# Kernel tuning notes

Hardware: AMD Instinct MI355X
Metric: run time of the kernel (lower is better)

## Reference

```python
import jax, jax.numpy as jnp
from jax import lax
import numpy as np

DIM, HEADS, R = 256, 8, 2
B, H, W = 4, 64, 64
C = DIM // HEADS
SCALE = C ** -0.5


def setup_inputs() -> dict:
    key = jax.random.key(0)
    ks = jax.random.split(key, 6)
    s = 0.02
    x = jax.random.normal(ks[0], (B, DIM, H, W), dtype=jnp.float32)
    Wq = jax.random.normal(ks[1], (DIM, DIM), dtype=jnp.float32) * s
    Wkv = jax.random.normal(ks[2], (2 * DIM, DIM, R, R), dtype=jnp.float32) * s
    Wqb = jax.random.normal(ks[3], (DIM, DIM), dtype=jnp.float32) * s
    Wkvb = jax.random.normal(ks[4], (2 * DIM, DIM), dtype=jnp.float32) * s
    Wout = jax.random.normal(ks[5], (DIM, DIM), dtype=jnp.float32) * s
    return {"x": x, "Wq": Wq, "Wkv": Wkv, "Wqb": Wqb, "Wkvb": Wkvb, "Wout": Wout}


def _conv1x1(Wm, t):
    # 1x1 conv without bias == channel matmul
    return jnp.einsum('oc,bchw->bohw', Wm, t)


def reference(x, Wq, Wkv, Wqb, Wkvb, Wout):
    b, d, h, w = x.shape
    c = d // HEADS
    # ---- spatial-reduction branch ----
    q = _conv1x1(Wq, x)  # [b, d, h, w]
    kv = lax.conv_general_dilated(x, Wkv, (R, R), 'VALID',
                                  dimension_numbers=('NCHW', 'OIHW', 'NCHW'))
    k, v = jnp.split(kv, 2, axis=1)  # each [b, d, h/R, w/R]

    def to_img(t):
        bb, _, hh, ww = t.shape
        return t.reshape(bb, HEADS, c, hh * ww).transpose(0, 1, 3, 2).reshape(bb * HEADS, hh * ww, c)

    qi, ki, vi = to_img(q), to_img(k), to_img(v)
    attn_img = jax.nn.softmax(jnp.einsum('bid,bjd->bij', qi, ki) * SCALE, axis=-1)
    oi = jnp.einsum('bij,bjd->bid', attn_img, vi)  # [(b h), hw, c]
    out_img = oi.reshape(b, HEADS, h * w, c).transpose(0, 1, 3, 2).reshape(b, d, h, w)

    # ---- batch-wise branch ----
    qb = _conv1x1(Wqb, x)
    kvb = _conv1x1(Wkvb, x)
    kb, vb = jnp.split(kvb, 2, axis=1)

    def to_slice(t):
        # 'b (h c) x y -> (x y h) b c'
        return t.reshape(b, HEADS, c, h * w).transpose(3, 1, 0, 2).reshape(h * w * HEADS, b, c)

    qs, ks_, vs = to_slice(qb), to_slice(kb), to_slice(vb)
    attn_b = jax.nn.softmax(jnp.einsum('ibd,icd->ibc', qs, ks_) * SCALE, axis=-1)
    ob = jnp.einsum('ibc,icd->ibd', attn_b, vs)  # [(hw heads), b, c]
    out_batch = ob.reshape(h * w, HEADS, b, c).transpose(2, 1, 3, 0).reshape(b, d, h, w)

    return _conv1x1(Wout, out_img + out_batch)
```

## Files before the change

### kernel.cpp

```cpp
#include <hip/hip_runtime.h>

#define ATTN_SCALE 0.17677669529663687f

typedef __attribute__((ext_vector_type(8))) short bf16x8;
typedef __attribute__((ext_vector_type(4))) float f32x4;
typedef __attribute__((ext_vector_type(16))) float f32x16;

__device__ inline unsigned short f2bf(float x) {
    unsigned int u = __float_as_uint(x);
    unsigned int r = u + 0x7fffu + ((u >> 16) & 1u);
    return (unsigned short)(r >> 16);
}
__device__ inline unsigned int pk2(float lo, float hi) {
    return (unsigned int)f2bf(lo) | ((unsigned int)f2bf(hi) << 16);
}
__device__ inline float bf2f(unsigned int u) { return __uint_as_float(u << 16); }

#define GLDS16(gp, lp) \
    __builtin_amdgcn_global_load_lds((const __attribute__((address_space(1))) void*)(gp), \
                                     (__attribute__((address_space(3))) void*)(lp), 16, 0, 0)

template<int NIT>
__device__ inline void stage_tile_n(const ushort* __restrict__ g, int rstride, int kofs,
                                    ushort* lbase, int w, int lane) {
    const int r0 = w * (NIT * 8);
    #pragma unroll
    for (int u = 0; u < NIT; ++u) {
        const int row  = r0 + u * 8 + (lane >> 3);
        const int slog = (lane & 7) ^ (row & 7);
        GLDS16(g + (size_t)row * rstride + kofs + slog * 8,
               lbase + (size_t)(r0 + u * 8) * 64);
    }
}
__device__ inline void stage_tile(const ushort* __restrict__ g, int rstride, int kofs,
                                  ushort* lbase, int w, int lane) {
    stage_tile_n<4>(g, rstride, kofs, lbase, w, lane);
}

__device__ inline bf16x8 frag_ld(const ushort* t, int row, int slog) {
    return *(const bf16x8*)(t + row * 64 + ((slog ^ (row & 7)) * 8));
}

#define MFMA_STEP(WS_, XS_, WM_, WP_)                                                       \
    _Pragma("unroll")                                                                       \
    for (int kh = 0; kh < 2; ++kh) {                                                        \
        bf16x8 av[4], bvv[4];                                                               \
        _Pragma("unroll")                                                                   \
        for (int fm = 0; fm < 4; ++fm) av[fm]  = frag_ld(WS_, WM_ + fm * 16 + i16, kh * 4 + g); \
        _Pragma("unroll")                                                                   \
        for (int fp = 0; fp < 4; ++fp) bvv[fp] = frag_ld(XS_, WP_ + fp * 16 + i16, kh * 4 + g); \
        _Pragma("unroll")                                                                   \
        for (int fm = 0; fm < 4; ++fm)                                                      \
            _Pragma("unroll")                                                               \
            for (int fp = 0; fp < 4; ++fp)                                                  \
                acc[fm][fp] = __builtin_amdgcn_mfma_f32_16x16x32_bf16(av[fm], bvv[fp],      \
                                                                      acc[fm][fp], 0, 0, 0); \
    }

__global__ __launch_bounds__(256) void cvt_x_fused(
    const float* __restrict__ x, ushort* __restrict__ xbfT, ushort* __restrict__ xcol)
{
    __shared__ float T[128][65];
    const int t  = threadIdx.x;
    const int i2 = blockIdx.x;
    const int c0 = blockIdx.y * 64, bb = blockIdx.z;
    const int p0 = i2 * 128;
    const float* xb = x + ((size_t)bb * 256 + c0) * 4096 + p0;

    {
        const int cc = t >> 2;
        const int pq = (t & 3) * 32;
        #pragma unroll
        for (int u = 0; u < 8; ++u) {
            const float4 v = *(const float4*)&xb[(size_t)cc * 4096 + pq + u * 4];
            T[pq + u * 4 + 0][cc] = v.x; T[pq + u * 4 + 1][cc] = v.y;
            T[pq + u * 4 + 2][cc] = v.z; T[pq + u * 4 + 3][cc] = v.w;
        }
    }
    __syncthreads();

    {
        const int pp = t >> 1, ch = (t & 1) * 32;
        const float* row = &T[pp][ch];
        unsigned int pkv[16];
        #pragma unroll
        for (int u = 0; u < 16; ++u) pkv[u] = pk2(row[2 * u], row[2 * u + 1]);
        ushort* dst = xbfT + ((size_t)bb * 4096 + p0 + pp) * 256 + c0 + ch;
        *(uint4*)&dst[0]  = *(uint4*)&pkv[0];
        *(uint4*)&dst[8]  = *(uint4*)&pkv[4];
        *(uint4*)&dst[16] = *(uint4*)&pkv[8];
        *(uint4*)&dst[24] = *(uint4*)&pkv[12];
    }
    {
        const int j = t >> 3, c8 = (t & 7) * 8;
        unsigned int pkv[16];
        #pragma unroll
        for (int c = 0; c < 8; ++c) {
            pkv[2 * c]     = pk2(T[2 * j][c8 + c],      T[2 * j + 1][c8 + c]);
            pkv[2 * c + 1] = pk2(T[64 + 2 * j][c8 + c], T[65 + 2 * j][c8 + c]);
        }
        ushort* dst = xcol + ((size_t)bb * 1024 + i2 * 32 + j) * 1024 + (size_t)(c0 + c8) * 4;
        *(uint4*)&dst[0]  = *(uint4*)&pkv[0];
        *(uint4*)&dst[8]  = *(uint4*)&pkv[4];
        *(uint4*)&dst[16] = *(uint4*)&pkv[8];
        *(uint4*)&dst[24] = *(uint4*)&pkv[12];
    }
}

__global__ __launch_bounds__(256) void cvt_w_kernel(
    const float* __restrict__ Wq, const float* __restrict__ Wqb,
    const float* __restrict__ Wkvb, const float* __restrict__ Wkv,
    const float* __restrict__ Wout,
    ushort* __restrict__ Wallb, ushort* __restrict__ Wkvbb, ushort* __restrict__ Woutb)
{
    const int id = blockIdx.x * 256 + threadIdx.x;
    const float* src; ushort* dst;
    if (id < 65536) {
        const int m = id >> 6, c4 = (id & 63) * 4;
        src = (m < 256) ? &Wq[(size_t)m * 256 + c4]
            : (m < 512) ? &Wqb[(size_t)(m - 256) * 256 + c4]
                        : &Wkvb[(size_t)(m - 512) * 256 + c4];
        dst = Wallb + (size_t)id * 4;
    } else if (id < 65536 + 131072) {
        const size_t el = (size_t)(id - 65536) * 4;
        src = &Wkv[el]; dst = Wkvbb + el;
    } else if (id < 65536 + 131072 + 16384) {
        const size_t el = (size_t)(id - 65536 - 131072) * 4;
        src = &Wout[el]; dst = Woutb + el;
    } else return;
    const float4 v = *(const float4*)src;
    ushort4 o; o.x = f2bf(v.x); o.y = f2bf(v.y); o.z = f2bf(v.z); o.w = f2bf(v.w);
    *(ushort4*)dst = o;
}

__global__ __launch_bounds__(256) void proj_mfma(
    const ushort* __restrict__ Wallb, const ushort* __restrict__ xbfT,
    ushort* __restrict__ qTb, ushort* __restrict__ qbT, ushort* __restrict__ kvbT)
{
    __shared__ __align__(16) ushort lds[16384];
    ushort* Ws = lds; ushort* Xs = lds + 8192;
    const int tid = threadIdx.x, lane = tid & 63, w = tid >> 6;
    const int g = lane >> 4, i16 = lane & 15;
    const int p0 = blockIdx.x * 128, m0 = blockIdx.y * 128, bb = blockIdx.z;
    const int wm = (w >> 1) * 64, wp = (w & 1) * 64;
    const ushort* Ag = Wallb + (size_t)m0 * 256;
    const ushort* Bg = xbfT + ((size_t)bb * 4096 + p0) * 256;
    f32x4 acc[4][4] = {};
    for (int ks = 0; ks < 4; ++ks) {
        stage_tile(Ag, 256, ks * 64, Ws, w, lane);
        stage_tile(Bg, 256, ks * 64, Xs, w, lane);
        __syncthreads();
        MFMA_STEP(Ws, Xs, wm, wp);
        __syncthreads();
    }
    #pragma unroll
    for (int fp = 0; fp < 4; ++fp) {
        const int p = p0 + wp + fp * 16 + i16;
        #pragma unroll
        for (int fm = 0; fm < 4; ++fm) {
            const int m = m0 + wm + fm * 16 + 4 * g;
            if (m0 < 256) {
                ushort4 v;
                v.x = f2bf(acc[fm][fp][0] * ATTN_SCALE); v.y = f2bf(acc[fm][fp][1] * ATTN_SCALE);
                v.z = f2bf(acc[fm][fp][2] * ATTN_SCALE); v.w = f2bf(acc[fm][fp][3] * ATTN_SCALE);
                *(ushort4*)&qTb[((size_t)bb * 4096 + p) * 256 + m] = v;
            } else if (m0 < 512) {
                ushort4 v;
                v.x = f2bf(acc[fm][fp][0]); v.y = f2bf(acc[fm][fp][1]);
                v.z = f2bf(acc[fm][fp][2]); v.w = f2bf(acc[fm][fp][3]);
                *(ushort4*)&qbT[((size_t)bb * 4096 + p) * 256 + (m - 256)] = v;
            } else {
                ushort4 v;
                v.x = f2bf(acc[fm][fp][0]); v.y = f2bf(acc[fm][fp][1]);
                v.z = f2bf(acc[fm][fp][2]); v.w = f2bf(acc[fm][fp][3]);
                *(ushort4*)&kvbT[((size_t)bb * 4096 + p) * 512 + (m - 512)] = v;
            }
        }
    }
}

__global__ __launch_bounds__(256) void conv_mfma(
    const ushort* __restrict__ Wkvbb, const ushort* __restrict__ xcol,
    ushort* __restrict__ kTb, ushort* __restrict__ vTtb)
{
    __shared__ __align__(16) ushort lds[12288];
    ushort* Ws = lds;
    ushort* Xs = lds + 4096;
    const int tid = threadIdx.x, lane = tid & 63, w = tid >> 6;
    const int g = lane >> 4, i16 = lane & 15;
    const int pp0 = blockIdx.x * 128, m0 = blockIdx.y * 64, bb = blockIdx.z;
    const int wm = (w >> 1) * 32, wp = (w & 1) * 64;
    const ushort* Ag = Wkvbb + (size_t)m0 * 1024;
    const ushort* Bg = xcol + ((size_t)bb * 1024 + pp0) * 1024;
    f32x4 acc[2][4] = {};
    for (int ks = 0; ks < 16; ++ks) {
        stage_tile_n<2>(Ag, 1024, ks * 64, Ws, w, lane);
        stage_tile_n<4>(Bg, 1024, ks * 64, Xs, w, lane);
        __syncthreads();
        #pragma unroll
        for (int kh = 0; kh < 2; ++kh) {
            bf16x8 av[2], bvv[4];
            #pragma unroll
            for (int fm = 0; fm < 2; ++fm) av[fm]  = frag_ld(Ws, wm + fm * 16 + i16, kh * 4 + g);
            #pragma unroll
            for (int fp = 0; fp < 4; ++fp) bvv[fp] = frag_ld(Xs, wp + fp * 16 + i16, kh * 4 + g);
            #pragma unroll
            for (int fm = 0; fm < 2; ++fm)
                #pragma unroll
                for (int fp = 0; fp < 4; ++fp)
                    acc[fm][fp] = __builtin_amdgcn_mfma_f32_16x16x32_bf16(av[fm], bvv[fp],
                                                                          acc[fm][fp], 0, 0, 0);
        }
        __syncthreads();
    }
    if (m0 < 256) {
        #pragma unroll
        for (int fp = 0; fp < 4; ++fp) {
            const int pp = pp0 + wp + fp * 16 + i16;
            #pragma unroll
            for (int fm = 0; fm < 2; ++fm) {
                const int m = m0 + wm + fm * 16 + 4 * g;
                ushort4 v;
                v.x = f2bf(acc[fm][fp][0]); v.y = f2bf(acc[fm][fp][1]);
                v.z = f2bf(acc[fm][fp][2]); v.w = f2bf(acc[fm][fp][3]);
                *(ushort4*)&kTb[((size_t)bb * 1024 + pp) * 256 + m] = v;
            }
        }
    } else {
        ushort (*T)[128] = (ushort(*)[128])lds;
        #pragma unroll
        for (int fm = 0; fm < 2; ++fm)
            #pragma unroll
            for (int fp = 0; fp < 4; ++fp)
                #pragma unroll
                for (int r = 0; r < 4; ++r)
                    T[wm + fm * 16 + 4 * g + r][wp + fp * 16 + i16] = f2bf(acc[fm][fp][r]);
        __syncthreads();
        #pragma unroll
        for (int u = 0; u < 4; ++u) {
            const int chunk = u * 256 + tid;
            const int row = chunk >> 4, slot = chunk & 15;
            const int mg = m0 - 256 + row;
            const int hh = mg >> 5, cc = mg & 31;
            const uint4 val = *(uint4*)&T[row][slot * 8];
            *(uint4*)&vTtb[((size_t)(bb * 8 + hh) * 32 + cc) * 1024 + pp0 + slot * 8] = val;
        }
    }
}

__global__ __launch_bounds__(256) void out_mfma(
    const float* __restrict__ sumT, const ushort* __restrict__ Woutb,
    float* __restrict__ out)
{
    __shared__ __align__(16) ushort lds[16384];
    ushort* Ss = lds; ushort* Wo = lds + 8192;
    const int tid = threadIdx.x, lane = tid & 63, w = tid >> 6;
    const int g = lane >> 4, i16 = lane & 15;
    const int p0 = blockIdx.x * 128, o0 = blockIdx.y * 128, bb = blockIdx.z;
    const int wpp = (w >> 1) * 64, wo = (w & 1) * 64;
    const float* Sg = sumT + ((size_t)bb * 4096 + p0) * 256;
    const ushort* Bgw = Woutb + (size_t)o0 * 256;
    const int srow = tid >> 1, shalf = tid & 1;
    f32x4 acc[4][4] = {};
    for (int ks = 0; ks < 4; ++ks) {
        {
            const float* src = Sg + (size_t)srow * 256 + ks * 64 + shalf * 32;
            #pragma unroll
            for (int jj = 0; jj < 4; ++jj) {
                const float4 f0 = *(const float4*)&src[jj * 8];
                const float4 f1 = *(const float4*)&src[jj * 8 + 4];
                uint4 pk;
                pk.x = pk2(f0.x, f0.y); pk.y = pk2(f0.z, f0.w);
                pk.z = pk2(f1.x, f1.y); pk.w = pk2(f1.z, f1.w);
                const int slog = shalf * 4 + jj;
                const int sp = slog ^ (srow & 7);
                *(uint4*)&Ss[(size_t)srow * 64 + sp * 8] = pk;
            }
        }
        stage_tile(Bgw, 256, ks * 64, Wo, w, lane);
        __syncthreads();
        MFMA_STEP(Ss, Wo, wpp, wo);
        __syncthreads();
    }
    #pragma unroll
    for (int fo = 0; fo < 4; ++fo) {
        const int o = o0 + wo + fo * 16 + i16;
        #pragma unroll
        for (int fp = 0; fp < 4; ++fp) {
            const int p = p0 + wpp + fp * 16 + 4 * g;
            const float4 v = make_float4(acc[fp][fo][0], acc[fp][fo][1],
                                         acc[fp][fo][2], acc[fp][fo][3]);
            *(float4*)&out[(size_t)bb * 1048576 + (size_t)o * 4096 + p] = v;
        }
    }
}

__global__ __launch_bounds__(256) void attn_img_mfma(
    const ushort* __restrict__ qTb, const ushort* __restrict__ kTb,
    const ushort* __restrict__ vTtb, float* __restrict__ sumT)
{
    __shared__ ushort Ks[128][40];
    __shared__ ushort Vts[32][136];
    const int tid  = threadIdx.x;
    const int lane = tid & 63;
    const int wv   = tid >> 6;
    const int q    = lane & 31;
    const int hi   = lane >> 5;
    const int bh   = blockIdx.x;
    const int b    = bh >> 3, h = bh & 7;
    const int q0   = blockIdx.y * 128 + wv * 32;

    bf16x8 qf[2];
    #pragma unroll
    for (int mm = 0; mm < 2; ++mm)
        qf[mm] = *(const bf16x8*)(qTb + ((size_t)(b * 4096 + q0 + q) * 256 + h * 32 + mm * 16 + hi * 8));

    f32x16 o = {};
    float mrun = -3.0e38f, lrun = 0.f;

    const ushort* kg = kTb + (size_t)b * 1024 * 256 + h * 32;
    const ushort* vg = vTtb + (size_t)bh * 32 * 1024;

    for (int kv0 = 0; kv0 < 1024; kv0 += 128) {
        __syncthreads();
        #pragma unroll
        for (int u = 0; u < 2; ++u) {
            const int chunk = tid + u * 256;
            const int r = chunk >> 2, q4 = chunk & 3;
            *(uint4*)&Ks[r][q4 * 8] = *(const uint4*)(kg + (size_t)(kv0 + r) * 256 + q4 * 8);
            const int c = chunk >> 4, sseg = chunk & 15;
            *(uint4*)&Vts[c][sseg * 8] = *(const uint4*)(vg + (size_t)c * 1024 + kv0 + sseg * 8);
        }
        __syncthreads();

        f32x16 s[4];
        #pragma unroll
        for (int t = 0; t < 4; ++t) {
            const bf16x8 k0 = *(const bf16x8*)&Ks[t * 32 + q][hi * 8];
            const bf16x8 k1 = *(const bf16x8*)&Ks[t * 32 + q][16 + hi * 8];
            f32x16 acc = {};
            acc = __builtin_amdgcn_mfma_f32_32x32x16_bf16(k0, qf[0], acc, 0, 0, 0);
            acc = __builtin_amdgcn_mfma_f32_32x32x16_bf16(k1, qf[1], acc, 0, 0, 0);
            s[t] = acc;
        }
        float pmax = -3.0e38f;
        #pragma unroll
        for (int t = 0; t < 4; ++t)
            #pragma unroll
            for (int r = 0; r < 16; ++r) pmax = fmaxf(pmax, s[t][r]);
        {
            float a_ = pmax, b_ = pmax;
            asm volatile("v_permlane32_swap_b32 %0, %1" : "+v"(a_), "+v"(b_));
            pmax = fmaxf(a_, b_);
        }
        const float mnew  = fmaxf(mrun, pmax);
        const float alpha = __expf(mrun - mnew);
        mrun = mnew;
        float ls = 0.f;
        #pragma unroll
        for (int t = 0; t < 4; ++t)
            #pragma unroll
            for (int r = 0; r < 16; ++r) {
                const float p = __expf(s[t][r] - mnew);
                s[t][r] = p; ls += p;
            }
        {
            float a_ = ls, b_ = ls;
            asm volatile("v_permlane32_swap_b32 %0, %1" : "+v"(a_), "+v"(b_));
            ls = a_ + b_;
        }
        lrun = lrun * alpha + ls;
        #pragma unroll
        for (int r = 0; r < 16; ++r) o[r] *= alpha;

        #pragma unroll
        for (int t = 0; t < 4; ++t) {
            unsigned int W[4][2];
            #pragma unroll
            for (int u = 0; u < 4; ++u) {
                asm("v_cvt_pk_bf16_f32 %0, %1, %2"
                    : "=v"(W[u][0]) : "v"(s[t][4 * u + 0]), "v"(s[t][4 * u + 1]));
                asm("v_cvt_pk_bf16_f32 %0, %1, %2"
                    : "=v"(W[u][1]) : "v"(s[t][4 * u + 2]), "v"(s[t][4 * u + 3]));
            }
            #pragma unroll
            for (int mm = 0; mm < 2; ++mm) {
                unsigned int a0 = W[2 * mm][0], b0 = W[2 * mm + 1][0];
                unsigned int a1 = W[2 * mm][1], b1 = W[2 * mm + 1][1];
                asm volatile("v_permlane32_swap_b32 %0, %1" : "+v"(a0), "+v"(b0));
                asm volatile("v_permlane32_swap_b32 %0, %1" : "+v"(a1), "+v"(b1));
                unsigned int pw[4] = {a0, a1, b0, b1};
                const bf16x8 pf = *(const bf16x8*)pw;
                const bf16x8 vf = *(const bf16x8*)&Vts[q][t * 32 + mm * 16 + hi * 8];
                o = __builtin_amdgcn_mfma_f32_32x32x16_bf16(vf, pf, o, 0, 0, 0);
            }
        }
    }

    const float inv = 1.f / lrun;
    float* dst = sumT + (size_t)(b * 4096 + q0 + q) * 256 + h * 32 + hi * 4;
    #pragma unroll
    for (int u = 0; u < 4; ++u) {
        const float4 v = make_float4(o[4 * u + 0] * inv, o[4 * u + 1] * inv,
                                     o[4 * u + 2] * inv, o[4 * u + 3] * inv);
        *(float4*)&dst[u * 8] = v;
    }
}

__global__ __launch_bounds__(256) void attn_batch_kernel(
    const ushort* __restrict__ qbT, const ushort* __restrict__ kvbT,
    float* __restrict__ sumT)
{
    __shared__ __align__(16) ushort kvs[8 * 2088];
    const int tid = threadIdx.x;
    const int p0 = blockIdx.x * 8;

    #pragma unroll
    for (int u = 0; u < 8; ++u) {
        const int c = u * 256 + tid;
        const int p = c >> 8;
        const int r = c & 255;
        const int b2 = r >> 6, seg = r & 63;
        const uint4 val = *(const uint4*)(kvbT + ((size_t)(b2 * 4096 + p0 + p)) * 512 + seg * 8);
        *(uint4*)&kvs[p * 2088 + b2 * 520 + seg * 8] = val;
    }
    __syncthreads();

    const int b1 = tid & 3, h = (tid >> 2) & 7, pl = tid >> 5;
    const int p = p0 + pl;
    const ushort* kvp = kvs + pl * 2088;

    const uint4* q4p = (const uint4*)(qbT + ((size_t)b1 * 4096 + p) * 256 + h * 32);
    float q[32];
    #pragma unroll
    for (int i = 0; i < 4; ++i) {
        const uint4 t = q4p[i];
        q[8 * i + 0] = bf2f(t.x & 0xffffu) * ATTN_SCALE; q[8 * i + 1] = bf2f(t.x >> 16) * ATTN_SCALE;
        q[8 * i + 2] = bf2f(t.y & 0xffffu) * ATTN_SCALE; q[8 * i + 3] = bf2f(t.y >> 16) * ATTN_SCALE;
        q[8 * i + 4] = bf2f(t.z & 0xffffu) * ATTN_SCALE; q[8 * i + 5] = bf2f(t.z >> 16) * ATTN_SCALE;
        q[8 * i + 6] = bf2f(t.w & 0xffffu) * ATTN_SCALE; q[8 * i + 7] = bf2f(t.w >> 16) * ATTN_SCALE;
    }

    float s[4];
    #pragma unroll
    for (int b2 = 0; b2 < 4; ++b2) {
        const uint4* k4 = (const uint4*)(kvp + b2 * 520 + h * 32);
        float d = 0.f;
        #pragma unroll
        for (int i = 0; i < 4; ++i) {
            const uint4 w = k4[i];
            d += q[8 * i + 0] * bf2f(w.x & 0xffffu) + q[8 * i + 1] * bf2f(w.x >> 16);
            d += q[8 * i + 2] * bf2f(w.y & 0xffffu) + q[8 * i + 3] * bf2f(w.y >> 16);
            d += q[8 * i + 4] * bf2f(w.z & 0xffffu) + q[8 * i + 5] * bf2f(w.z >> 16);
            d += q[8 * i + 6] * bf2f(w.w & 0xffffu) + q[8 * i + 7] * bf2f(w.w >> 16);
        }
        s[b2] = d;
    }
    const float mx = fmaxf(fmaxf(s[0], s[1]), fmaxf(s[2], s[3]));
    float w[4];
    float lsum = 0.f;
    #pragma unroll
    for (int b2 = 0; b2 < 4; ++b2) { w[b2] = __expf(s[b2] - mx); lsum += w[b2]; }
    const float inv = 1.f / lsum;
    #pragma unroll
    for (int b2 = 0; b2 < 4; ++b2) w[b2] *= inv;

    float acc[32] = {};
    #pragma unroll
    for (int b2 = 0; b2 < 4; ++b2) {
        const uint4* v4 = (const uint4*)(kvp + b2 * 520 + 256 + h * 32);
        const float wb = w[b2];
        #pragma unroll
        for (int i = 0; i < 4; ++i) {
            const uint4 vv = v4[i];
            acc[8 * i + 0] += wb * bf2f(vv.x & 0xffffu); acc[8 * i + 1] += wb * bf2f(vv.x >> 16);
            acc[8 * i + 2] += wb * bf2f(vv.y & 0xffffu); acc[8 * i + 3] += wb * bf2f(vv.y >> 16);
            acc[8 * i + 4] += wb * bf2f(vv.z & 0xffffu); acc[8 * i + 5] += wb * bf2f(vv.z >> 16);
            acc[8 * i + 6] += wb * bf2f(vv.w & 0xffffu); acc[8 * i + 7] += wb * bf2f(vv.w >> 16);
        }
    }
    float4* o4 = (float4*)(sumT + ((size_t)b1 * 4096 + p) * 256 + h * 32);
    #pragma unroll
    for (int i = 0; i < 8; ++i) {
        float4 c = o4[i];
        c.x += acc[4 * i + 0]; c.y += acc[4 * i + 1];
        c.z += acc[4 * i + 2]; c.w += acc[4 * i + 3];
        o4[i] = c;
    }
}

extern "C" void kernel_launch(void* const* d_in, const int* in_sizes, int n_in,
                              void* d_out, int out_size, void* d_ws, size_t ws_size,
                              hipStream_t stream)
{
    const float* x    = (const float*)d_in[0];
    const float* Wq   = (const float*)d_in[1];
    const float* Wkv  = (const float*)d_in[2];
    const float* Wqb  = (const float*)d_in[3];
    const float* Wkvb = (const float*)d_in[4];
    const float* Wout = (const float*)d_in[5];
    float* out = (float*)d_out;

    ushort* base  = (ushort*)d_ws;
    ushort* xbfT  = base;
    ushort* xcol  = base + 4194304;
    ushort* Wallb = base + 8388608;
    ushort* Wkvbb = base + 8650752;
    float*  sumT  = (float*)base;
    ushort* qTb   = base + 9175040;
    ushort* kvbT  = base + 13369344;
    ushort* kTb   = base + 21757952;
    ushort* vTtb  = base + 22806528;
    ushort* Woutb = base + 23855104;
    ushort* qbT   = (ushort*)out;

    cvt_x_fused<<<dim3(32, 4, 4), 256, 0, stream>>>(x, xbfT, xcol);
    cvt_w_kernel<<<dim3(832), 256, 0, stream>>>(Wq, Wqb, Wkvb, Wkv, Wout, Wallb, Wkvbb, Woutb);
    proj_mfma<<<dim3(32, 8, 4), 256, 0, stream>>>(Wallb, xbfT, qTb, qbT, kvbT);
    conv_mfma<<<dim3(8, 8, 4), 256, 0, stream>>>(Wkvbb, xcol, kTb, vTtb);
    attn_img_mfma<<<dim3(32, 32), 256, 0, stream>>>(qTb, kTb, vTtb, sumT);
    attn_batch_kernel<<<dim3(512), 256, 0, stream>>>(qbT, kvbT, sumT);
    out_mfma<<<dim3(32, 2, 4), 256, 0, stream>>>(sumT, Woutb, out);
}
```

Before: 121.4 us.

## Merge image and batch attention into one launch, sum branches in output GEMM

The image-attention and batch-attention kernels become a single launch, with block index selecting the branch, so the two can run concurrently and the small batch kernel no longer runs alone at low occupancy. The batch branch now writes its output as bf16 to a separate buffer rather than doing a read-modify-write on the fp32 sum buffer. The output projection reads both buffers and adds them while staging. This removes one launch and the serial dependency between the two attention kernels. In exchange the output GEMM does extra loads, and the batch output is rounded to bf16 earlier.

```diff
diff --git a/kernel.cpp b/kernel.cpp
--- a/kernel.cpp
+++ b/kernel.cpp
@@ -249,8 +249,8 @@
 }
 
 __global__ __launch_bounds__(256) void out_mfma(
-    const float* __restrict__ sumT, const ushort* __restrict__ Woutb,
-    float* __restrict__ out)
+    const float* __restrict__ sumT, const ushort* __restrict__ obT,
+    const ushort* __restrict__ Woutb, float* __restrict__ out)
 {
     __shared__ __align__(16) ushort lds[16384];
     ushort* Ss = lds; ushort* Wo = lds + 8192;
@@ -259,19 +259,25 @@
     const int p0 = blockIdx.x * 128, o0 = blockIdx.y * 128, bb = blockIdx.z;
     const int wpp = (w >> 1) * 64, wo = (w & 1) * 64;
     const float* Sg = sumT + ((size_t)bb * 4096 + p0) * 256;
+    const ushort* Og = obT + ((size_t)bb * 4096 + p0) * 256;
     const ushort* Bgw = Woutb + (size_t)o0 * 256;
     const int srow = tid >> 1, shalf = tid & 1;
     f32x4 acc[4][4] = {};
     for (int ks = 0; ks < 4; ++ks) {
         {
             const float* src = Sg + (size_t)srow * 256 + ks * 64 + shalf * 32;
+            const ushort* osrc = Og + (size_t)srow * 256 + ks * 64 + shalf * 32;
             #pragma unroll
             for (int jj = 0; jj < 4; ++jj) {
                 const float4 f0 = *(const float4*)&src[jj * 8];
                 const float4 f1 = *(const float4*)&src[jj * 8 + 4];
+                const uint2 b0 = *(const uint2*)&osrc[jj * 8];
+                const uint2 b1 = *(const uint2*)&osrc[jj * 8 + 4];
                 uint4 pk;
-                pk.x = pk2(f0.x, f0.y); pk.y = pk2(f0.z, f0.w);
-                pk.z = pk2(f1.x, f1.y); pk.w = pk2(f1.z, f1.w);
+                pk.x = pk2(f0.x + bf2f(b0.x & 0xffffu), f0.y + bf2f(b0.x >> 16));
+                pk.y = pk2(f0.z + bf2f(b0.y & 0xffffu), f0.w + bf2f(b0.y >> 16));
+                pk.z = pk2(f1.x + bf2f(b1.x & 0xffffu), f1.y + bf2f(b1.x >> 16));
+                pk.w = pk2(f1.z + bf2f(b1.y & 0xffffu), f1.w + bf2f(b1.y >> 16));
                 const int slog = shalf * 4 + jj;
                 const int sp = slog ^ (srow & 7);
                 *(uint4*)&Ss[(size_t)srow * 64 + sp * 8] = pk;
@@ -295,197 +301,200 @@
     }
 }
 
-__global__ __launch_bounds__(256) void attn_img_mfma(
+__global__ __launch_bounds__(256) void attn_fused(
     const ushort* __restrict__ qTb, const ushort* __restrict__ kTb,
-    const ushort* __restrict__ vTtb, float* __restrict__ sumT)
-{
-    __shared__ ushort Ks[128][40];
-    __shared__ ushort Vts[32][136];
-    const int tid  = threadIdx.x;
-    const int lane = tid & 63;
-    const int wv   = tid >> 6;
-    const int q    = lane & 31;
-    const int hi   = lane >> 5;
-    const int bh   = blockIdx.x;
-    const int b    = bh >> 3, h = bh & 7;
-    const int q0   = blockIdx.y * 128 + wv * 32;
-
-    bf16x8 qf[2];
-    #pragma unroll
-    for (int mm = 0; mm < 2; ++mm)
-        qf[mm] = *(const bf16x8*)(qTb + ((size_t)(b * 4096 + q0 + q) * 256 + h * 32 + mm * 16 + hi * 8));
-
-    f32x16 o = {};
-    float mrun = -3.0e38f, lrun = 0.f;
-
-    const ushort* kg = kTb + (size_t)b * 1024 * 256 + h * 32;
-    const ushort* vg = vTtb + (size_t)bh * 32 * 1024;
-
-    for (int kv0 = 0; kv0 < 1024; kv0 += 128) {
-        __syncthreads();
-        #pragma unroll
-        for (int u = 0; u < 2; ++u) {
-            const int chunk = tid + u * 256;
-            const int r = chunk >> 2, q4 = chunk & 3;
-            *(uint4*)&Ks[r][q4 * 8] = *(const uint4*)(kg + (size_t)(kv0 + r) * 256 + q4 * 8);
-            const int c = chunk >> 4, sseg = chunk & 15;
-            *(uint4*)&Vts[c][sseg * 8] = *(const uint4*)(vg + (size_t)c * 1024 + kv0 + sseg * 8);
-        }
-        __syncthreads();
-
-        f32x16 s[4];
-        #pragma unroll
-        for (int t = 0; t < 4; ++t) {
-            const bf16x8 k0 = *(const bf16x8*)&Ks[t * 32 + q][hi * 8];
-            const bf16x8 k1 = *(const bf16x8*)&Ks[t * 32 + q][16 + hi * 8];
-            f32x16 acc = {};
-            acc = __builtin_amdgcn_mfma_f32_32x32x16_bf16(k0, qf[0], acc, 0, 0, 0);
-            acc = __builtin_amdgcn_mfma_f32_32x32x16_bf16(k1, qf[1], acc, 0, 0, 0);
-            s[t] = acc;
-        }
-        float pmax = -3.0e38f;
-        #pragma unroll
-        for (int t = 0; t < 4; ++t)
-            #pragma unroll
-            for (int r = 0; r < 16; ++r) pmax = fmaxf(pmax, s[t][r]);
-        {
-            float a_ = pmax, b_ = pmax;
-            asm volatile("v_permlane32_swap_b32 %0, %1" : "+v"(a_), "+v"(b_));
-            pmax = fmaxf(a_, b_);
-        }
-        const float mnew  = fmaxf(mrun, pmax);
-        const float alpha = __expf(mrun - mnew);
-        mrun = mnew;
-        float ls = 0.f;
-        #pragma unroll
-        for (int t = 0; t < 4; ++t)
-            #pragma unroll
-            for (int r = 0; r < 16; ++r) {
-                const float p = __expf(s[t][r] - mnew);
-                s[t][r] = p; ls += p;
-            }
-        {
-            float a_ = ls, b_ = ls;
-            asm volatile("v_permlane32_swap_b32 %0, %1" : "+v"(a_), "+v"(b_));
-            ls = a_ + b_;
-        }
-        lrun = lrun * alpha + ls;
-        #pragma unroll
-        for (int r = 0; r < 16; ++r) o[r] *= alpha;
-
-        #pragma unroll
-        for (int t = 0; t < 4; ++t) {
-            unsigned int W[4][2];
-            #pragma unroll
-            for (int u = 0; u < 4; ++u) {
-                asm("v_cvt_pk_bf16_f32 %0, %1, %2"
-                    : "=v"(W[u][0]) : "v"(s[t][4 * u + 0]), "v"(s[t][4 * u + 1]));
-                asm("v_cvt_pk_bf16_f32 %0, %1, %2"
-                    : "=v"(W[u][1]) : "v"(s[t][4 * u + 2]), "v"(s[t][4 * u + 3]));
-            }
-            #pragma unroll
-            for (int mm = 0; mm < 2; ++mm) {
-                unsigned int a0 = W[2 * mm][0], b0 = W[2 * mm + 1][0];
-                unsigned int a1 = W[2 * mm][1], b1 = W[2 * mm + 1][1];
-                asm volatile("v_permlane32_swap_b32 %0, %1" : "+v"(a0), "+v"(b0));
-                asm volatile("v_permlane32_swap_b32 %0, %1" : "+v"(a1), "+v"(b1));
-                unsigned int pw[4] = {a0, a1, b0, b1};
-                const bf16x8 pf = *(const bf16x8*)pw;
-                const bf16x8 vf = *(const bf16x8*)&Vts[q][t * 32 + mm * 16 + hi * 8];
-                o = __builtin_amdgcn_mfma_f32_32x32x16_bf16(vf, pf, o, 0, 0, 0);
-            }
-        }
-    }
-
-    const float inv = 1.f / lrun;
-    float* dst = sumT + (size_t)(b * 4096 + q0 + q) * 256 + h * 32 + hi * 4;
-    #pragma unroll
-    for (int u = 0; u < 4; ++u) {
-        const float4 v = make_float4(o[4 * u + 0] * inv, o[4 * u + 1] * inv,
-                                     o[4 * u + 2] * inv, o[4 * u + 3] * inv);
-        *(float4*)&dst[u * 8] = v;
-    }
-}
-
-__global__ __launch_bounds__(256) void attn_batch_kernel(
-    const ushort* __restrict__ qbT, const ushort* __restrict__ kvbT,
-    float* __restrict__ sumT)
-{
-    __shared__ __align__(16) ushort kvs[8 * 2088];
+    const ushort* __restrict__ vTtb, const ushort* __restrict__ qbT,
+    const ushort* __restrict__ kvbT, float* __restrict__ sumT,
+    ushort* __restrict__ obT)
+{
+    __shared__ __align__(16) ushort smem[16704];
+    const int bid = blockIdx.x;
     const int tid = threadIdx.x;
-    const int p0 = blockIdx.x * 8;
-
-    #pragma unroll
-    for (int u = 0; u < 8; ++u) {
-        const int c = u * 256 + tid;
-        const int p = c >> 8;
-        const int r = c & 255;
-        const int b2 = r >> 6, seg = r & 63;
-        const uint4 val = *(const uint4*)(kvbT + ((size_t)(b2 * 4096 + p0 + p)) * 512 + seg * 8);
-        *(uint4*)&kvs[p * 2088 + b2 * 520 + seg * 8] = val;
-    }
-    __syncthreads();
-
-    const int b1 = tid & 3, h = (tid >> 2) & 7, pl = tid >> 5;
-    const int p = p0 + pl;
-    const ushort* kvp = kvs + pl * 2088;
-
-    const uint4* q4p = (const uint4*)(qbT + ((size_t)b1 * 4096 + p) * 256 + h * 32);
-    float q[32];
-    #pragma unroll
-    for (int i = 0; i < 4; ++i) {
-        const uint4 t = q4p[i];
-        q[8 * i + 0] = bf2f(t.x & 0xffffu) * ATTN_SCALE; q[8 * i + 1] = bf2f(t.x >> 16) * ATTN_SCALE;
-        q[8 * i + 2] = bf2f(t.y & 0xffffu) * ATTN_SCALE; q[8 * i + 3] = bf2f(t.y >> 16) * ATTN_SCALE;
-        q[8 * i + 4] = bf2f(t.z & 0xffffu) * ATTN_SCALE; q[8 * i + 5] = bf2f(t.z >> 16) * ATTN_SCALE;
-        q[8 * i + 6] = bf2f(t.w & 0xffffu) * ATTN_SCALE; q[8 * i + 7] = bf2f(t.w >> 16) * ATTN_SCALE;
-    }
-
-    float s[4];
-    #pragma unroll
-    for (int b2 = 0; b2 < 4; ++b2) {
-        const uint4* k4 = (const uint4*)(kvp + b2 * 520 + h * 32);
-        float d = 0.f;
+
+    if (bid < 1024) {
+        ushort (*Ks)[40]  = (ushort(*)[40])smem;
+        ushort (*Vts)[136] = (ushort(*)[136])(smem + 5120);
+        const int lane = tid & 63;
+        const int wv   = tid >> 6;
+        const int q    = lane & 31;
+        const int hi   = lane >> 5;
+        const int bh   = bid >> 5;
+        const int b    = bh >> 3, h = bh & 7;
+        const int q0   = (bid & 31) * 128 + wv * 32;
+
+        bf16x8 qf[2];
+        #pragma unroll
+        for (int mm = 0; mm < 2; ++mm)
+            qf[mm] = *(const bf16x8*)(qTb + ((size_t)(b * 4096 + q0 + q) * 256 + h * 32 + mm * 16 + hi * 8));
+
+        f32x16 o = {};
+        float mrun = -3.0e38f, lrun = 0.f;
+
+        const ushort* kg = kTb + (size_t)b * 1024 * 256 + h * 32;
+        const ushort* vg = vTtb + (size_t)bh * 32 * 1024;
+
+        for (int kv0 = 0; kv0 < 1024; kv0 += 128) {
+            __syncthreads();
+            #pragma unroll
+            for (int u = 0; u < 2; ++u) {
+                const int chunk = tid + u * 256;
+                const int r = chunk >> 2, q4 = chunk & 3;
+                *(uint4*)&Ks[r][q4 * 8] = *(const uint4*)(kg + (size_t)(kv0 + r) * 256 + q4 * 8);
+                const int c = chunk >> 4, sseg = chunk & 15;
+                *(uint4*)&Vts[c][sseg * 8] = *(const uint4*)(vg + (size_t)c * 1024 + kv0 + sseg * 8);
+            }
+            __syncthreads();
+
+            f32x16 s[4];
+            #pragma unroll
+            for (int t = 0; t < 4; ++t) {
+                const bf16x8 k0 = *(const bf16x8*)&Ks[t * 32 + q][hi * 8];
+                const bf16x8 k1 = *(const bf16x8*)&Ks[t * 32 + q][16 + hi * 8];
+                f32x16 acc = {};
+                acc = __builtin_amdgcn_mfma_f32_32x32x16_bf16(k0, qf[0], acc, 0, 0, 0);
+                acc = __builtin_amdgcn_mfma_f32_32x32x16_bf16(k1, qf[1], acc, 0, 0, 0);
+                s[t] = acc;
+            }
+            float pmax = -3.0e38f;
+            #pragma unroll
+            for (int t = 0; t < 4; ++t)
+                #pragma unroll
+                for (int r = 0; r < 16; ++r) pmax = fmaxf(pmax, s[t][r]);
+            {
+                float a_ = pmax, b_ = pmax;
+                asm volatile("v_permlane32_swap_b32 %0, %1" : "+v"(a_), "+v"(b_));
+                pmax = fmaxf(a_, b_);
+            }
+            const float mnew  = fmaxf(mrun, pmax);
+            const float alpha = __expf(mrun - mnew);
+            mrun = mnew;
+            float ls = 0.f;
+            #pragma unroll
+            for (int t = 0; t < 4; ++t)
+                #pragma unroll
+                for (int r = 0; r < 16; ++r) {
+                    const float p = __expf(s[t][r] - mnew);
+                    s[t][r] = p; ls += p;
+                }
+            {
+                float a_ = ls, b_ = ls;
+                asm volatile("v_permlane32_swap_b32 %0, %1" : "+v"(a_), "+v"(b_));
+                ls = a_ + b_;
+            }
+            lrun = lrun * alpha + ls;
+            #pragma unroll
+            for (int r = 0; r < 16; ++r) o[r] *= alpha;
+
+            #pragma unroll
+            for (int t = 0; t < 4; ++t) {
+                unsigned int W[4][2];
+                #pragma unroll
+                for (int u = 0; u < 4; ++u) {
+                    asm("v_cvt_pk_bf16_f32 %0, %1, %2"
+                        : "=v"(W[u][0]) : "v"(s[t][4 * u + 0]), "v"(s[t][4 * u + 1]));
+                    asm("v_cvt_pk_bf16_f32 %0, %1, %2"
+                        : "=v"(W[u][1]) : "v"(s[t][4 * u + 2]), "v"(s[t][4 * u + 3]));
+                }
+                #pragma unroll
+                for (int mm = 0; mm < 2; ++mm) {
+                    unsigned int a0 = W[2 * mm][0], b0 = W[2 * mm + 1][0];
+                    unsigned int a1 = W[2 * mm][1], b1 = W[2 * mm + 1][1];
+                    asm volatile("v_permlane32_swap_b32 %0, %1" : "+v"(a0), "+v"(b0));
+                    asm volatile("v_permlane32_swap_b32 %0, %1" : "+v"(a1), "+v"(b1));
+                    unsigned int pw[4] = {a0, a1, b0, b1};
+                    const bf16x8 pf = *(const bf16x8*)pw;
+                    const bf16x8 vf = *(const bf16x8*)&Vts[q][t * 32 + mm * 16 + hi * 8];
+                    o = __builtin_amdgcn_mfma_f32_32x32x16_bf16(vf, pf, o, 0, 0, 0);
+                }
+            }
+        }
+
+        const float inv = 1.f / lrun;
+        float* dst = sumT + (size_t)(b * 4096 + q0 + q) * 256 + h * 32 + hi * 4;
+        #pragma unroll
+        for (int u = 0; u < 4; ++u) {
+            const float4 v = make_float4(o[4 * u + 0] * inv, o[4 * u + 1] * inv,
+                                         o[4 * u + 2] * inv, o[4 * u + 3] * inv);
+            *(float4*)&dst[u * 8] = v;
+        }
+    } else {
+        ushort* kvs = smem;
+        const int p0 = (bid - 1024) * 8;
+
+        #pragma unroll
+        for (int u = 0; u < 8; ++u) {
+            const int c = u * 256 + tid;
+            const int p = c >> 8;
+            const int r = c & 255;
+            const int b2 = r >> 6, seg = r & 63;
+            const uint4 val = *(const uint4*)(kvbT + ((size_t)(b2 * 4096 + p0 + p)) * 512 + seg * 8);
+            *(uint4*)&kvs[p * 2088 + b2 * 520 + seg * 8] = val;
+        }
+        __syncthreads();
+
+        const int b1 = tid & 3, h = (tid >> 2) & 7, pl = tid >> 5;
+        const int p = p0 + pl;
+        const ushort* kvp = kvs + pl * 2088;
+
+        const uint4* q4p = (const uint4*)(qbT + ((size_t)b1 * 4096 + p) * 256 + h * 32);
+        float q[32];
         #pragma unroll
         for (int i = 0; i < 4; ++i) {
-            const uint4 w = k4[i];
-            d += q[8 * i + 0] * bf2f(w.x & 0xffffu) + q[8 * i + 1] * bf2f(w.x >> 16);
-            d += q[8 * i + 2] * bf2f(w.y & 0xffffu) + q[8 * i + 3] * bf2f(w.y >> 16);
-            d += q[8 * i + 4] * bf2f(w.z & 0xffffu) + q[8 * i + 5] * bf2f(w.z >> 16);
-            d += q[8 * i + 6] * bf2f(w.w & 0xffffu) + q[8 * i + 7] * bf2f(w.w >> 16);
-        }
-        s[b2] = d;
-    }
-    const float mx = fmaxf(fmaxf(s[0], s[1]), fmaxf(s[2], s[3]));
-    float w[4];
-    float lsum = 0.f;
-    #pragma unroll
-    for (int b2 = 0; b2 < 4; ++b2) { w[b2] = __expf(s[b2] - mx); lsum += w[b2]; }
-    const float inv = 1.f / lsum;
-    #pragma unroll
-    for (int b2 = 0; b2 < 4; ++b2) w[b2] *= inv;
-
-    float acc[32] = {};
-    #pragma unroll
-    for (int b2 = 0; b2 < 4; ++b2) {
-        const uint4* v4 = (const uint4*)(kvp + b2 * 520 + 256 + h * 32);
-        const float wb = w[b2];
+            const uint4 t = q4p[i];
+            q[8 * i + 0] = bf2f(t.x & 0xffffu) * ATTN_SCALE; q[8 * i + 1] = bf2f(t.x >> 16) * ATTN_SCALE;
+            q[8 * i + 2] = bf2f(t.y & 0xffffu) * ATTN_SCALE; q[8 * i + 3] = bf2f(t.y >> 16) * ATTN_SCALE;
+            q[8 * i + 4] = bf2f(t.z & 0xffffu) * ATTN_SCALE; q[8 * i + 5] = bf2f(t.z >> 16) * ATTN_SCALE;
+            q[8 * i + 6] = bf2f(t.w & 0xffffu) * ATTN_SCALE; q[8 * i + 7] = bf2f(t.w >> 16) * ATTN_SCALE;
+        }
+
+        float s[4];
+        #pragma unroll
+        for (int b2 = 0; b2 < 4; ++b2) {
+            const uint4* k4 = (const uint4*)(kvp + b2 * 520 + h * 32);
+            float d = 0.f;
+            #pragma unroll
+            for (int i = 0; i < 4; ++i) {
+                const uint4 w = k4[i];
+                d += q[8 * i + 0] * bf2f(w.x & 0xffffu) + q[8 * i + 1] * bf2f(w.x >> 16);
+                d += q[8 * i + 2] * bf2f(w.y & 0xffffu) + q[8 * i + 3] * bf2f(w.y >> 16);
+                d += q[8 * i + 4] * bf2f(w.z & 0xffffu) + q[8 * i + 5] * bf2f(w.z >> 16);
+                d += q[8 * i + 6] * bf2f(w.w & 0xffffu) + q[8 * i + 7] * bf2f(w.w >> 16);
+            }
+            s[b2] = d;
+        }
+        const float mx = fmaxf(fmaxf(s[0], s[1]), fmaxf(s[2], s[3]));
+        float w[4];
+        float lsum = 0.f;
+        #pragma unroll
+        for (int b2 = 0; b2 < 4; ++b2) { w[b2] = __expf(s[b2] - mx); lsum += w[b2]; }
+        const float inv = 1.f / lsum;
+        #pragma unroll
+        for (int b2 = 0; b2 < 4; ++b2) w[b2] *= inv;
+
+        float acc[32] = {};
+        #pragma unroll
+        for (int b2 = 0; b2 < 4; ++b2) {
+            const uint4* v4 = (const uint4*)(kvp + b2 * 520 + 256 + h * 32);
+            const float wb = w[b2];
+            #pragma unroll
+            for (int i = 0; i < 4; ++i) {
+                const uint4 vv = v4[i];
+                acc[8 * i + 0] += wb * bf2f(vv.x & 0xffffu); acc[8 * i + 1] += wb * bf2f(vv.x >> 16);
+                acc[8 * i + 2] += wb * bf2f(vv.y & 0xffffu); acc[8 * i + 3] += wb * bf2f(vv.y >> 16);
+                acc[8 * i + 4] += wb * bf2f(vv.z & 0xffffu); acc[8 * i + 5] += wb * bf2f(vv.z >> 16);
+                acc[8 * i + 6] += wb * bf2f(vv.w & 0xffffu); acc[8 * i + 7] += wb * bf2f(vv.w >> 16);
+            }
+        }
+        uint4* o4 = (uint4*)(obT + ((size_t)b1 * 4096 + p) * 256 + h * 32);
         #pragma unroll
         for (int i = 0; i < 4; ++i) {
-            const uint4 vv = v4[i];
-            acc[8 * i + 0] += wb * bf2f(vv.x & 0xffffu); acc[8 * i + 1] += wb * bf2f(vv.x >> 16);
-            acc[8 * i + 2] += wb * bf2f(vv.y & 0xffffu); acc[8 * i + 3] += wb * bf2f(vv.y >> 16);
-            acc[8 * i + 4] += wb * bf2f(vv.z & 0xffffu); acc[8 * i + 5] += wb * bf2f(vv.z >> 16);
-            acc[8 * i + 6] += wb * bf2f(vv.w & 0xffffu); acc[8 * i + 7] += wb * bf2f(vv.w >> 16);
-        }
-    }
-    float4* o4 = (float4*)(sumT + ((size_t)b1 * 4096 + p) * 256 + h * 32);
-    #pragma unroll
-    for (int i = 0; i < 8; ++i) {
-        float4 c = o4[i];
-        c.x += acc[4 * i + 0]; c.y += acc[4 * i + 1];
-        c.z += acc[4 * i + 2]; c.w += acc[4 * i + 3];
-        o4[i] = c;
+            uint4 r;
+            r.x = pk2(acc[8 * i + 0], acc[8 * i + 1]);
+            r.y = pk2(acc[8 * i + 2], acc[8 * i + 3]);
+            r.z = pk2(acc[8 * i + 4], acc[8 * i + 5]);
+            r.w = pk2(acc[8 * i + 6], acc[8 * i + 7]);
+            o4[i] = r;
+        }
     }
 }
 
@@ -512,13 +521,13 @@
     ushort* kTb   = base + 21757952;
     ushort* vTtb  = base + 22806528;
     ushort* Woutb = base + 23855104;
+    ushort* obT   = base + 23920640;
     ushort* qbT   = (ushort*)out;
 
     cvt_x_fused<<<dim3(32, 4, 4), 256, 0, stream>>>(x, xbfT, xcol);
     cvt_w_kernel<<<dim3(832), 256, 0, stream>>>(Wq, Wqb, Wkvb, Wkv, Wout, Wallb, Wkvbb, Woutb);
     proj_mfma<<<dim3(32, 8, 4), 256, 0, stream>>>(Wallb, xbfT, qTb, qbT, kvbT);
     conv_mfma<<<dim3(8, 8, 4), 256, 0, stream>>>(Wkvbb, xcol, kTb, vTtb);
-    attn_img_mfma<<<dim3(32, 32), 256, 0, stream>>>(qTb, kTb, vTtb, sumT);
-    attn_batch_kernel<<<dim3(512), 256, 0, stream>>>(qbT, kvbT, sumT);
-    out_mfma<<<dim3(32, 2, 4), 256, 0, stream>>>(sumT, Woutb, out);
-}
+    attn_fused<<<dim3(1536), 256, 0, stream>>>(qTb, kTb, vTtb, qbT, kvbT, sumT, obT);
+    out_mfma<<<dim3(32, 2, 4), 256, 0, stream>>>(sumT, obT, Woutb, out);
+}
```

Measured after the change: 112.8 us (median of 2 runs). 7.1% less time.
